# Performance work log

Hardware: AMD Instinct MI355X
Metric: run time of the kernel (lower is better)

## Reference

```python
import jax, jax.numpy as jnp
import numpy as np

B, CIN, H, W = 4, 512, 63, 63
CI, CO = 256, 512  # dim_inter, dim_out
K = 9              # adaptive pool output size; H % K == 0 so pool is exact 7x7 avg
BN_EPS = 1e-5


def conv1x1(x, w, b):
    # x: [B,C,H,W], w: [O,C], b: [O]
    return jnp.einsum('bchw,oc->bohw', x, w) + b[None, :, None, None]


def bn_eval(x, gamma, beta):
    # eval-mode BatchNorm2d with running_mean=0, running_var=1
    s = gamma / jnp.sqrt(jnp.asarray(1.0 + BN_EPS, x.dtype))
    return x * s[None, :, None, None] + beta[None, :, None, None]


def setup_inputs() -> dict:
    key = jax.random.key(0)
    ks = jax.random.split(key, 11)
    sc = 0.02
    return {
        'data_input': jax.random.normal(ks[0], (B, CIN, H, W), jnp.float32),
        'Wk': jax.random.normal(ks[1], (CI, CIN), jnp.float32) * sc,
        'bk': jnp.zeros((CI,), jnp.float32),
        'gamma': 1.0 + 0.1 * jax.random.normal(ks[2], (CI,), jnp.float32),
        'beta': 0.1 * jax.random.normal(ks[3], (CI,), jnp.float32),
        'Wv': jax.random.normal(ks[4], (CI, CIN), jnp.float32) * sc,
        'bv': jnp.zeros((CI,), jnp.float32),
        'Wv2': jax.random.normal(ks[5], (CI, CI), jnp.float32) * sc,
        'bv2': jnp.zeros((CI,), jnp.float32),
        'Ww': jax.random.normal(ks[6], (CO, CI), jnp.float32) * sc,  # note: torch init is 0; randomized for a non-trivial baseline
        'bw': jnp.zeros((CO,), jnp.float32),
    }


def reference(data_input, Wk, bk, gamma, beta, Wv, bv, Wv2, bv2, Ww, bw):
    x = data_input
    scale = jnp.asarray(CI ** (-0.5), x.dtype)

    value = conv1x1(x, Wv, bv)                       # [B,CI,H,W]
    # AdaptiveAvgPool2d(9) with H,W divisible by 9 -> exact block average
    v2 = value.reshape(B, CI, K, H // K, K, W // K).mean(axis=(3, 5))  # [B,CI,9,9]
    v2 = conv1x1(v2, Wv2, bv2).reshape(B, CI, K * K)  # [B,CI,81]

    qk = bn_eval(conv1x1(x, Wk, bk), gamma, beta).reshape(B, CI, -1)  # shared query/key [B,CI,N]
    v = value.reshape(B, CI, -1)                      # [B,CI,N]

    # sim_map = softmax(Q^T K / sqrt(C)) over keys -> [B,N,N]
    sim = jax.nn.softmax(jnp.einsum('bcn,bcm->bnm', qk, qk) * scale, axis=-1)
    # sim_map_value = softmax(V^T V2 / sqrt(C)) -> [B,N,81]
    simv = jax.nn.softmax(jnp.einsum('bcn,bck->bnk', v, v2) * scale, axis=-1)

    sim_new = jnp.einsum('bnm,bmk->bnk', sim, simv)   # [B,N,81]
    ctx = jnp.einsum('bnk,bck->bcn', sim_new, v2).reshape(B, CI, H, W)
    return conv1x1(ctx, Ww, bw)                       # [B,CO,H,W]
```

## Files before the change

### kernel.cpp

```cpp
#include <hip/hip_runtime.h>
#include <hip/hip_bf16.h>

#define BB 4
#define CINsz 512
#define HH 63
#define NN 3969
#define NPAD 4032
#define NPAD2 4096
#define CI 256
#define CO 512
#define NK 81
#define NKP 96
#define SCALE 0.0625f
#define BN_EPS 1e-5f
#define NSPLIT 4

typedef __bf16 bf16x8 __attribute__((ext_vector_type(8)));
typedef float f32x4 __attribute__((ext_vector_type(4)));
typedef unsigned short us8 __attribute__((ext_vector_type(8)));
typedef unsigned short us4 __attribute__((ext_vector_type(4)));

#define MFMA16(a, b, c) __builtin_amdgcn_mfma_f32_16x16x32_bf16((a), (b), (c), 0, 0, 0)

__device__ inline unsigned short f2bf(float x) {
    union { float f; unsigned int u; } v; v.f = x;
    unsigned int r = v.u + 0x7FFF + ((v.u >> 16) & 1);
    return (unsigned short)(r >> 16);
}
__device__ inline float bf2f(unsigned short u) {
    union { unsigned int u; float f; } v; v.u = ((unsigned int)u) << 16;
    return v.f;
}

__device__ inline void gll16(const void* g, void* l) {
    __builtin_amdgcn_global_load_lds(
        (const __attribute__((address_space(1))) unsigned int*)g,
        (__attribute__((address_space(3))) unsigned int*)l, 16, 0, 0);
}

__global__ __launch_bounds__(256) void k_prep(
    const float* __restrict__ Wk, const float* __restrict__ bk,
    const float* __restrict__ gamma, const float* __restrict__ beta,
    const float* __restrict__ Wv, const float* __restrict__ bv,
    const float* __restrict__ Wv2, const float* __restrict__ Ww,
    unsigned short* __restrict__ Wkv, float* __restrict__ bias2,
    unsigned short* __restrict__ Wv2b, unsigned short* __restrict__ Wwb,
    unsigned short* __restrict__ qkbf)
{
    int idx = blockIdx.x * 256 + threadIdx.x;
    if (idx < 512 * 512) {
        int o = idx >> 9, c = idx & 511;
        float v;
        if (o < 256) { float s = gamma[o] * rsqrtf(1.f + BN_EPS); v = Wk[(size_t)o * 512 + c] * s; }
        else v = Wv[(size_t)(o - 256) * 512 + c];
        Wkv[idx] = f2bf(v);
        if (c == 0) {
            bias2[o] = (o < 256) ? (bk[o] * (gamma[o] * rsqrtf(1.f + BN_EPS)) + beta[o]) : bv[o - 256];
        }
    } else if (idx < 512 * 512 + 256 * 256) {
        int j = idx - 512 * 512;
        Wv2b[j] = f2bf(Wv2[j]);
    } else if (idx < 512 * 512 + 256 * 256 + 512 * 256) {
        int j = idx - 512 * 512 - 256 * 256;
        Wwb[j] = f2bf(Ww[j]);
    } else if (idx < 512 * 512 + 256 * 256 + 512 * 256 + 8192) {
        int j = idx - (512 * 512 + 256 * 256 + 512 * 256);
        int b = j >> 11, rem = j & 2047;
        us8 z = (us8){0, 0, 0, 0, 0, 0, 0, 0};
        *reinterpret_cast<us8*>(&qkbf[(size_t)b * NPAD2 * CI + (size_t)NPAD * CI + rem * 8]) = z;
    }
}

__global__ __launch_bounds__(256) void k_qkv(const float* __restrict__ x,
                                             const unsigned short* __restrict__ Wkv,
                                             const float* __restrict__ bias2,
                                             unsigned short* __restrict__ qkbf,
                                             unsigned short* __restrict__ value)
{
    int b = blockIdx.y;
    int nbase = blockIdx.x * 32;
    int tid = threadIdx.x, w = tid >> 6, lane = tid & 63, lg = lane >> 4, lr = lane & 15;
    int half = w >> 1;
    int o_off = half * 256;
    int nloc = (w & 1) * 16 + lr;

    __shared__ unsigned short xs[256 * 34];
    __shared__ unsigned short wk[512 * 32];

    f32x4 acc[16];
#pragma unroll
    for (int t = 0; t < 16; ++t) acc[t] = (f32x4){0.f, 0.f, 0.f, 0.f};

    int n_l = tid & 31, cg = tid >> 5;
    int n_g = nbase + n_l;
    bool nok = n_g < NN;

    for (int h = 0; h < 2; ++h) {
        __syncthreads();
        const float* xsrc = x + ((size_t)b * CINsz + h * 256 + cg) * NN + n_g;
#pragma unroll
        for (int i = 0; i < 32; ++i) {
            int cl = cg + i * 8;
            xs[cl * 34 + n_l] = nok ? f2bf(xsrc[(size_t)(i * 8) * NN]) : (unsigned short)0;
        }
        for (int s8 = 0; s8 < 8; ++s8) {
            int c0 = (h * 8 + s8) * 32;
            __syncthreads();
#pragma unroll
            for (int j = 0; j < 8; ++j) {
                int o = w * 128 + j * 16 + (lane >> 2);
                int slot = (lane & 3) ^ (o & 3);
                gll16(Wkv + (size_t)o * CINsz + c0 + slot * 8,
                      &wk[(w * 128 + j * 16) * 32]);
            }
            __syncthreads();
            bf16x8 af;
#pragma unroll
            for (int j2 = 0; j2 < 8; ++j2)
                af[j2] = __builtin_bit_cast(__bf16, xs[(s8 * 32 + lg * 8 + j2) * 34 + nloc]);
            __builtin_amdgcn_s_setprio(1);
#pragma unroll
            for (int t = 0; t < 16; ++t) {
                int o_loc = o_off + t * 16 + lr;
                bf16x8 bf = *reinterpret_cast<const bf16x8*>(
                    &wk[o_loc * 32 + ((lg ^ (o_loc & 3)) << 3)]);
                acc[t] = MFMA16(af, bf, acc[t]);
            }
            __builtin_amdgcn_s_setprio(0);
        }
    }
    if (half == 0) {
        unsigned short* dst = qkbf + (size_t)b * NPAD2 * CI;
#pragma unroll
        for (int t = 0; t < 16; ++t) {
            int o = t * 16 + lr;
            float bsum = bias2[o];
#pragma unroll
            for (int r = 0; r < 4; ++r) {
                int n = nbase + (w & 1) * 16 + lg * 4 + r;
                dst[(size_t)n * CI + o] = f2bf((acc[t][r] + bsum) * 0.25f);
            }
        }
    } else {
        unsigned short* dst = value + (size_t)b * NPAD * CI;
#pragma unroll
        for (int t = 0; t < 16; ++t) {
            int o = t * 16 + lr;
            float bsum = bias2[256 + o];
#pragma unroll
            for (int r = 0; r < 4; ++r) {
                int n = nbase + (w & 1) * 16 + lg * 4 + r;
                dst[(size_t)n * CI + o] = f2bf(acc[t][r] + bsum);
            }
        }
    }
}

__global__ __launch_bounds__(256) void k_pool(const unsigned short* __restrict__ value,
                                              unsigned short* __restrict__ pooled)
{
    int b = blockIdx.y, k = blockIdx.x, c = threadIdx.x;
    unsigned short* dst = pooled + ((size_t)b * NKP + k) * CI + c;
    if (k >= NK) { *dst = 0; return; }
    int ky = k / 9, kx = k % 9;
    const unsigned short* vb = value + (size_t)b * NPAD * CI + c;
    float s = 0.f;
#pragma unroll
    for (int y = 0; y < 7; ++y)
#pragma unroll
        for (int xx = 0; xx < 7; ++xx) {
            int n = (ky * 7 + y) * HH + kx * 7 + xx;
            s += bf2f(vb[(size_t)n * CI]);
        }
    *dst = f2bf(s * (1.f / 49.f));
}

__global__ __launch_bounds__(256) void k_v2(const unsigned short* __restrict__ pooled,
                                            const unsigned short* __restrict__ Wv2b,
                                            const float* __restrict__ bv2,
                                            unsigned short* __restrict__ v2f)
{
    int b = blockIdx.y;
    int tid = threadIdx.x, w = tid >> 6, lane = tid & 63, lg = lane >> 4, lr = lane & 15;
    int ot = blockIdx.x * 4 + w;
    const unsigned short* pb = pooled + (size_t)b * NKP * CI + lg * 8;
    const unsigned short* wb = Wv2b + (size_t)(ot * 16 + lr) * CI + lg * 8;
    f32x4 acc[6];
#pragma unroll
    for (int kt = 0; kt < 6; ++kt) acc[kt] = (f32x4){0.f, 0.f, 0.f, 0.f};
#pragma unroll
    for (int s = 0; s < 8; ++s) {
        bf16x8 bfw = *reinterpret_cast<const bf16x8*>(wb + s * 32);
#pragma unroll
        for (int kt = 0; kt < 6; ++kt) {
            bf16x8 af = *reinterpret_cast<const bf16x8*>(pb + (size_t)(kt * 16 + lr) * CI + s * 32);
            acc[kt] = MFMA16(af, bfw, acc[kt]);
        }
    }
    float bias = bv2[ot * 16 + lr];
#pragma unroll
    for (int kt = 0; kt < 6; ++kt)
#pragma unroll
        for (int r = 0; r < 4; ++r)
            v2f[((size_t)b * NKP + kt * 16 + lg * 4 + r) * CI + ot * 16 + lr] = f2bf(acc[kt][r] + bias);
}

__global__ __launch_bounds__(256) void k_Z(const unsigned short* __restrict__ Wwb,
                                           const unsigned short* __restrict__ v2f,
                                           unsigned short* __restrict__ Zt)
{
    int b = blockIdx.y;
    int tid = threadIdx.x, w = tid >> 6, lane = tid & 63, lg = lane >> 4, lr = lane & 15;
    int ot = blockIdx.x * 4 + w;
    const unsigned short* wb = Wwb + (size_t)(ot * 16 + lr) * CI + lg * 8;
    const unsigned short* vb = v2f + (size_t)b * NKP * CI + lg * 8;
    f32x4 acc[6];
#pragma unroll
    for (int kt = 0; kt < 6; ++kt) acc[kt] = (f32x4){0.f, 0.f, 0.f, 0.f};
#pragma unroll
    for (int s = 0; s < 8; ++s) {
        bf16x8 af = *reinterpret_cast<const bf16x8*>(wb + s * 32);
#pragma unroll
        for (int kt = 0; kt < 6; ++kt) {
            bf16x8 bfv = *reinterpret_cast<const bf16x8*>(vb + (size_t)(kt * 16 + lr) * CI + s * 32);
            acc[kt] = MFMA16(af, bfv, acc[kt]);
        }
    }
#pragma unroll
    for (int kt = 0; kt < 6; ++kt)
#pragma unroll
        for (int r = 0; r < 4; ++r)
            Zt[((size_t)b * CO + ot * 16 + lg * 4 + r) * NKP + kt * 16 + lr] = f2bf(acc[kt][r]);
}

__global__ __launch_bounds__(256) void k_simv(const unsigned short* __restrict__ value,
                                              const unsigned short* __restrict__ v2f,
                                              unsigned short* __restrict__ svT)
{
    int b = blockIdx.y;
    int tid = threadIdx.x, w = tid >> 6, lane = tid & 63, lg = lane >> 4, lr = lane & 15;
    int n0 = blockIdx.x * 64 + w * 16;

    __shared__ unsigned short sv[96 * 256];

    const unsigned short* v2base = v2f + (size_t)b * NKP * CI;
#pragma unroll
    for (int j = 0; j < 12; ++j) {
        int L = w * 12 + j;
        int row = 2 * L + (lane >> 5);
        int c_hw = ((lane & 31) * 8) ^ ((row & 7) << 3);
        gll16(v2base + (size_t)row * CI + c_hw, &sv[2 * L * 256]);
    }
    __syncthreads();

    const unsigned short* vrow = value + ((size_t)b * NPAD + n0 + lr) * CI + lg * 8;
    f32x4 acc[6];
#pragma unroll
    for (int kt = 0; kt < 6; ++kt) acc[kt] = (f32x4){0.f, 0.f, 0.f, 0.f};
#pragma unroll
    for (int s = 0; s < 8; ++s) {
        bf16x8 af = *reinterpret_cast<const bf16x8*>(vrow + s * 32);
        __builtin_amdgcn_s_setprio(1);
#pragma unroll
        for (int kt = 0; kt < 6; ++kt) {
            int row = kt * 16 + lr;
            bf16x8 bfv = *reinterpret_cast<const bf16x8*>(
                &sv[row * 256 + ((s * 32 + lg * 8) ^ ((row & 7) << 3))]);
            acc[kt] = MFMA16(af, bfv, acc[kt]);
        }
        __builtin_amdgcn_s_setprio(0);
    }
#pragma unroll
    for (int kt = 0; kt < 6; ++kt) {
        bool bad = (kt * 16 + lr) >= NK;
#pragma unroll
        for (int r = 0; r < 4; ++r) acc[kt][r] = bad ? -1e30f : acc[kt][r] * SCALE;
    }
#pragma unroll
    for (int r = 0; r < 4; ++r) {
        float m = acc[0][r];
#pragma unroll
        for (int kt = 1; kt < 6; ++kt) m = fmaxf(m, acc[kt][r]);
#pragma unroll
        for (int off = 1; off < 16; off <<= 1) m = fmaxf(m, __shfl_xor(m, off));
        float p[6], sum = 0.f;
#pragma unroll
        for (int kt = 0; kt < 6; ++kt) { p[kt] = __expf(acc[kt][r] - m); sum += p[kt]; }
#pragma unroll
        for (int off = 1; off < 16; off <<= 1) sum += __shfl_xor(sum, off);
        float inv = 1.f / sum;
#pragma unroll
        for (int kt = 0; kt < 6; ++kt) acc[kt][r] = p[kt] * inv;
    }
#pragma unroll
    for (int kt = 0; kt < 6; ++kt) {
        us4 pk;
#pragma unroll
        for (int r = 0; r < 4; ++r) pk[r] = f2bf(acc[kt][r]);
        if (kt * 16 + lr == 81) { pk[0] = pk[1] = pk[2] = pk[3] = 0x3F80; }
        *reinterpret_cast<us4*>(&svT[((size_t)b * NKP + kt * 16 + lr) * NPAD + n0 + lg * 4]) = pk;
    }
}

__global__ __launch_bounds__(256, 2) void k_flash(const unsigned short* __restrict__ qkbf,
                                                  const unsigned short* __restrict__ svT,
                                                  unsigned short* __restrict__ part_acc,
                                                  float* __restrict__ part_ml)
{
    int bid = blockIdx.x;
    int b = bid & 3;
    int rest = bid >> 2;
    int qg = rest & 31;
    int s_id = rest >> 5;
    int lo = s_id * 16;
    int hi = lo + 16 > 63 ? 63 : lo + 16;
    int tid = threadIdx.x, w = tid >> 6, lane = tid & 63, lg = lane >> 4, lr = lane & 15;
    int q0 = qg * 128 + w * 16;

    __shared__ unsigned short k_lds[2][64 * 256];
    __shared__ unsigned short sv_lds[96 * 64];

    const unsigned short* qkb = qkbf + (size_t)b * NPAD2 * CI;
    const unsigned short* svb = svT + (size_t)b * NKP * NPAD;

    bf16x8 qa[2][8];
#pragma unroll
    for (int u = 0; u < 2; ++u)
#pragma unroll
        for (int s = 0; s < 8; ++s)
            qa[u][s] = *reinterpret_cast<const bf16x8*>(
                qkb + (size_t)(q0 + u * 64 + lr) * CI + s * 32 + lg * 8);

    f32x4 acc[2][6];
#pragma unroll
    for (int u = 0; u < 2; ++u)
#pragma unroll
        for (int jt = 0; jt < 6; ++jt) acc[u][jt] = (f32x4){0.f, 0.f, 0.f, 0.f};
    float m_run[2][4];
#pragma unroll
    for (int u = 0; u < 2; ++u)
#pragma unroll
        for (int r = 0; r < 4; ++r) m_run[u][r] = -1e30f;

    auto stageK = [&](int t, int bi) {
#pragma unroll
        for (int j = 0; j < 8; ++j) {
            int r = w * 16 + j * 2 + (lane >> 5);
            int c_hw = ((lane & 31) * 8) ^ ((r & 7) << 3);
            gll16(qkb + (size_t)(t * 64 + r) * CI + c_hw,
                  &k_lds[bi][(w * 16 + j * 2) * 256]);
        }
    };
    auto stageSV = [&](int t) {
#pragma unroll
        for (int j = 0; j < 3; ++j) {
            int k = w * 24 + j * 8 + (lane >> 3);
            int m_hw = ((lane & 7) * 8) ^ ((k & 7) << 3);
            gll16(svb + (size_t)k * NPAD + t * 64 + m_hw,
                  &sv_lds[(w * 24 + j * 8) * 64]);
        }
    };

    stageK(lo, 0);
    stageSV(lo);
    __syncthreads();

    for (int t = lo; t < hi; ++t) {
        int bi = (t - lo) & 1;
        int mbase = t * 64;
        if (t + 1 < hi) stageK(t + 1, bi ^ 1);

        f32x4 s_acc[2][4];
#pragma unroll
        for (int u = 0; u < 2; ++u)
#pragma unroll
            for (int tt = 0; tt < 4; ++tt) s_acc[u][tt] = (f32x4){0.f, 0.f, 0.f, 0.f};
        __builtin_amdgcn_s_setprio(1);
#pragma unroll
        for (int s = 0; s < 8; ++s) {
            bf16x8 kf[4];
#pragma unroll
            for (int tt = 0; tt < 4; ++tt) {
                int row = tt * 16 + lr;
                int hw = (s * 32 + lg * 8) ^ ((row & 7) << 3);
                kf[tt] = *reinterpret_cast<const bf16x8*>(&k_lds[bi][row * 256 + hw]);
            }
#pragma unroll
            for (int tt = 0; tt < 4; ++tt) {
                s_acc[0][tt] = MFMA16(qa[0][s], kf[tt], s_acc[0][tt]);
                s_acc[1][tt] = MFMA16(qa[1][s], kf[tt], s_acc[1][tt]);
            }
        }
        __builtin_amdgcn_s_setprio(0);
        __syncthreads();

        unsigned short* pw = &k_lds[bi][w * 2048];
        bool lastTile = (mbase + 64 > NN);
#pragma unroll
        for (int u = 0; u < 2; ++u) {
            if (lastTile) {
#pragma unroll
                for (int tt = 0; tt < 4; ++tt) {
                    bool bad = (mbase + tt * 16 + lr) >= NN;
#pragma unroll
                    for (int r = 0; r < 4; ++r) if (bad) s_acc[u][tt][r] = -1e30f;
                }
            }
            float pmax[4];
#pragma unroll
            for (int r = 0; r < 4; ++r) {
                float m0 = fmaxf(fmaxf(s_acc[u][0][r], s_acc[u][1][r]),
                                 fmaxf(s_acc[u][2][r], s_acc[u][3][r]));
#pragma unroll
                for (int off = 1; off < 16; off <<= 1) m0 = fmaxf(m0, __shfl_xor(m0, off));
                pmax[r] = m0;
            }
            bool ok = (pmax[0] - m_run[u][0] <= 8.f) && (pmax[1] - m_run[u][1] <= 8.f) &&
                      (pmax[2] - m_run[u][2] <= 8.f) && (pmax[3] - m_run[u][3] <= 8.f);
            if (!__all(ok)) {
#pragma unroll
                for (int r = 0; r < 4; ++r) {
                    float mn = fmaxf(m_run[u][r], pmax[r]);
                    float al = __expf(m_run[u][r] - mn);
                    m_run[u][r] = mn;
#pragma unroll
                    for (int jt = 0; jt < 6; ++jt) acc[u][jt][r] *= al;
                }
            }
            unsigned short* pu = pw + u * 1024;
#pragma unroll
            for (int tt = 0; tt < 4; ++tt) {
#pragma unroll
                for (int r = 0; r < 4; ++r) {
                    float p = __expf(s_acc[u][tt][r] - m_run[u][r]);
                    int row = lg * 4 + r, col = tt * 16 + lr;
                    pu[row * 64 + (col ^ ((row & 7) << 3))] = f2bf(p);
                }
            }
        }
        __builtin_amdgcn_s_setprio(1);
#pragma unroll
        for (int kb = 0; kb < 2; ++kb) {
            int hw = kb * 32 + lg * 8;
            int phw = hw ^ ((lr & 7) << 3);
            bf16x8 pa0 = *reinterpret_cast<const bf16x8*>(&pw[lr * 64 + phw]);
            bf16x8 pa1 = *reinterpret_cast<const bf16x8*>(&pw[1024 + lr * 64 + phw]);
#pragma unroll
            for (int jt = 0; jt < 6; ++jt) {
                int cr = jt * 16 + lr;
                bf16x8 svf = *reinterpret_cast<const bf16x8*>(
                    &sv_lds[cr * 64 + (hw ^ ((cr & 7) << 3))]);
                acc[0][jt] = MFMA16(pa0, svf, acc[0][jt]);
                acc[1][jt] = MFMA16(pa1, svf, acc[1][jt]);
            }
        }
        __builtin_amdgcn_s_setprio(0);
        __syncthreads();
        if (t + 1 < hi) stageSV(t + 1);
    }
    int plane = s_id * 4 + b;
    unsigned short* pa_out = part_acc + (size_t)plane * NPAD2 * 96;
    float* ml_out = part_ml + (size_t)plane * 2 * NPAD2;
#pragma unroll
    for (int u = 0; u < 2; ++u)
#pragma unroll
        for (int r = 0; r < 4; ++r) {
            int row = q0 + u * 64 + lg * 4 + r;
#pragma unroll
            for (int jt = 0; jt < 6; ++jt)
                pa_out[(size_t)row * 96 + jt * 16 + lr] = f2bf(acc[u][jt][r]);
            if (lr == 0) ml_out[row] = m_run[u][r];
            if (lr == 1) ml_out[NPAD2 + row] = acc[u][5][r];
        }
}

__global__ __launch_bounds__(256) void k_out(const unsigned short* __restrict__ part_acc,
                                             const float* __restrict__ part_ml,
                                             const unsigned short* __restrict__ Zt,
                                             const float* __restrict__ bw,
                                             float* __restrict__ out)
{
    int b = blockIdx.y;
    int ng = blockIdx.x;
    int tid = threadIdx.x, w = tid >> 6, lane = tid & 63, lg = lane >> 4, lr = lane & 15;

    __shared__ unsigned short sn[64 * 104];

    for (int j = tid; j < 768; j += 256) {
        int row_l = j / 12, ch = j - row_l * 12;
        int row = ng * 64 + row_l;
        float m_s[NSPLIT], l_s[NSPLIT];
        float mg = -1e30f;
#pragma unroll
        for (int s = 0; s < NSPLIT; ++s) {
            const float* ml = part_ml + (size_t)(s * 4 + b) * 2 * NPAD2;
            m_s[s] = ml[row]; l_s[s] = ml[NPAD2 + row];
            mg = fmaxf(mg, m_s[s]);
        }
        float f_s[NSPLIT], denom = 0.f;
#pragma unroll
        for (int s = 0; s < NSPLIT; ++s) { f_s[s] = __expf(m_s[s] - mg); denom += f_s[s] * l_s[s]; }
        float inv = 1.f / denom;
        float a[8];
#pragma unroll
        for (int q = 0; q < 8; ++q) a[q] = 0.f;
#pragma unroll
        for (int s = 0; s < NSPLIT; ++s) {
            us8 v = *reinterpret_cast<const us8*>(
                &part_acc[((size_t)(s * 4 + b) * NPAD2 + row) * 96 + ch * 8]);
#pragma unroll
            for (int q = 0; q < 8; ++q) a[q] += f_s[s] * bf2f(v[q]);
        }
        us8 o;
#pragma unroll
        for (int q = 0; q < 8; ++q) o[q] = f2bf(a[q] * inv);
        if (ch == 10) o[1] = 0;
        *reinterpret_cast<us8*>(&sn[row_l * 104 + ch * 8]) = o;
    }
    __syncthreads();

    for (int og = 0; og < 8; ++og) {
        int o_row = (og * 4 + w) * 16;
        const unsigned short* za = Zt + ((size_t)b * CO + o_row + lr) * NKP + lg * 8;
        bf16x8 az[3];
#pragma unroll
        for (int ks = 0; ks < 3; ++ks) az[ks] = *reinterpret_cast<const bf16x8*>(za + ks * 32);
        f32x4 acc[4];
#pragma unroll
        for (int jn = 0; jn < 4; ++jn) acc[jn] = (f32x4){0.f, 0.f, 0.f, 0.f};
#pragma unroll
        for (int jn = 0; jn < 4; ++jn)
#pragma unroll
            for (int ks = 0; ks < 3; ++ks) {
                bf16x8 bfs = *reinterpret_cast<const bf16x8*>(
                    &sn[(jn * 16 + lr) * 104 + ks * 32 + lg * 8]);
                acc[jn] = MFMA16(az[ks], bfs, acc[jn]);
            }
#pragma unroll
        for (int r = 0; r < 4; ++r) {
            int o = o_row + lg * 4 + r;
            float bias = bw[o];
            float* orow = out + ((size_t)b * CO + o) * NN;
#pragma unroll
            for (int jn = 0; jn < 4; ++jn) {
                int n = ng * 64 + jn * 16 + lr;
                if (n < NN) orow[n] = acc[jn][r] + bias;
            }
        }
    }
}

extern "C" void kernel_launch(void* const* d_in, const int* in_sizes, int n_in,
                              void* d_out, int out_size, void* d_ws, size_t ws_size,
                              hipStream_t stream)
{
    const float* x     = (const float*)d_in[0];
    const float* Wk    = (const float*)d_in[1];
    const float* bk    = (const float*)d_in[2];
    const float* gamma = (const float*)d_in[3];
    const float* beta  = (const float*)d_in[4];
    const float* Wv    = (const float*)d_in[5];
    const float* bv    = (const float*)d_in[6];
    const float* Wv2   = (const float*)d_in[7];
    const float* bv2   = (const float*)d_in[8];
    const float* Ww    = (const float*)d_in[9];
    const float* bw    = (const float*)d_in[10];
    float* out = (float*)d_out;

    char* p = (char*)d_ws;
    unsigned short* qkbf   = (unsigned short*)p; p += (size_t)BB * NPAD2 * CI * 2;
    unsigned short* value  = (unsigned short*)p; p += (size_t)BB * NPAD * CI * 2;
    unsigned short* svT    = (unsigned short*)p; p += (size_t)BB * NKP * NPAD * 2;
    unsigned short* Wkv    = (unsigned short*)p; p += (size_t)512 * 512 * 2;
    unsigned short* Wv2b   = (unsigned short*)p; p += (size_t)256 * 256 * 2;
    unsigned short* Wwb    = (unsigned short*)p; p += (size_t)512 * 256 * 2;
    unsigned short* pooled = (unsigned short*)p; p += (size_t)BB * NKP * CI * 2;
    unsigned short* v2f    = (unsigned short*)p; p += (size_t)BB * NKP * CI * 2;
    unsigned short* Zt     = (unsigned short*)p; p += (size_t)BB * CO * NKP * 2;
    float* bias2           = (float*)p;          p += 512 * 4;
    unsigned short* part_acc = (unsigned short*)p; p += (size_t)16 * NPAD2 * 96 * 2;
    float* part_ml         = (float*)p;          p += (size_t)16 * 2 * NPAD2 * 4;

    k_prep<<<dim3(1826), 256, 0, stream>>>(Wk, bk, gamma, beta, Wv, bv, Wv2, Ww,
                                           Wkv, bias2, Wv2b, Wwb, qkbf);
    k_qkv<<<dim3(126, BB), 256, 0, stream>>>(x, Wkv, bias2, qkbf, value);
    k_pool<<<dim3(NKP, BB), 256, 0, stream>>>(value, pooled);
    k_v2<<<dim3(4, BB), 256, 0, stream>>>(pooled, Wv2b, bv2, v2f);
    k_Z<<<dim3(8, BB), 256, 0, stream>>>(Wwb, v2f, Zt);
    k_simv<<<dim3(63, BB), 256, 0, stream>>>(value, v2f, svT);
    k_flash<<<dim3(512), 256, 0, stream>>>(qkbf, svT, part_acc, part_ml);
    k_out<<<dim3(63, BB), 256, 0, stream>>>(part_acc, part_ml, Zt, bw, out);
}
```

Measured before the change: 158.2 us.

## Single-buffer K tile in LDS with register prefetch to fit three blocks per CU

The flash kernel drops its double-buffered K tile in LDS for a single buffer. The next K tile is now prefetched into registers and written to LDS after the P·V stage, with explicit waitcnt and barrier placement. This cuts LDS per block from about 76KB to 44KB, so launch bounds can rise to 3 blocks per CU for more latency hiding. The cost is 32 extra VGPRs held across the QK compute under a tighter register cap, which risks spills. It also adds an extra LDS write and barrier per tile and a redundant load on the last iteration.

```diff
diff --git a/kernel.cpp b/kernel.cpp
--- a/kernel.cpp
+++ b/kernel.cpp
@@ -302,7 +302,7 @@
     }
 }
 
-__global__ __launch_bounds__(256, 2) void k_flash(const unsigned short* __restrict__ qkbf,
+__global__ __launch_bounds__(256, 3) void k_flash(const unsigned short* __restrict__ qkbf,
                                                   const unsigned short* __restrict__ svT,
                                                   unsigned short* __restrict__ part_acc,
                                                   float* __restrict__ part_ml)
@@ -317,8 +317,8 @@
     int tid = threadIdx.x, w = tid >> 6, lane = tid & 63, lg = lane >> 4, lr = lane & 15;
     int q0 = qg * 128 + w * 16;
 
-    __shared__ unsigned short k_lds[2][64 * 256];
-    __shared__ unsigned short sv_lds[96 * 64];
+    __shared__ __align__(16) unsigned short k_lds[64 * 256];
+    __shared__ __align__(16) unsigned short sv_lds[96 * 64];
 
     const unsigned short* qkb = qkbf + (size_t)b * NPAD2 * CI;
     const unsigned short* svb = svT + (size_t)b * NKP * NPAD;
@@ -342,33 +342,31 @@
 #pragma unroll
         for (int r = 0; r < 4; ++r) m_run[u][r] = -1e30f;
 
-    auto stageK = [&](int t, int bi) {
+#pragma unroll
+    for (int j = 0; j < 8; ++j) {
+        int r = w * 16 + j * 2 + (lane >> 5);
+        int c_hw = ((lane & 31) * 8) ^ ((r & 7) << 3);
+        gll16(qkb + (size_t)(lo * 64 + r) * CI + c_hw, &k_lds[(w * 16 + j * 2) * 256]);
+    }
+#pragma unroll
+    for (int j = 0; j < 3; ++j) {
+        int k = w * 24 + j * 8 + (lane >> 3);
+        int m_hw = ((lane & 7) * 8) ^ ((k & 7) << 3);
+        gll16(svb + (size_t)k * NPAD + lo * 64 + m_hw, &sv_lds[(w * 24 + j * 8) * 64]);
+    }
+    __syncthreads();
+
+    for (int t = lo; t < hi; ++t) {
+        int mbase = t * 64;
+        int tn = (t + 1 < hi) ? t + 1 : hi - 1;
+
+        us8 kreg[8];
 #pragma unroll
         for (int j = 0; j < 8; ++j) {
             int r = w * 16 + j * 2 + (lane >> 5);
             int c_hw = ((lane & 31) * 8) ^ ((r & 7) << 3);
-            gll16(qkb + (size_t)(t * 64 + r) * CI + c_hw,
-                  &k_lds[bi][(w * 16 + j * 2) * 256]);
-        }
-    };
-    auto stageSV = [&](int t) {
-#pragma unroll
-        for (int j = 0; j < 3; ++j) {
-            int k = w * 24 + j * 8 + (lane >> 3);
-            int m_hw = ((lane & 7) * 8) ^ ((k & 7) << 3);
-            gll16(svb + (size_t)k * NPAD + t * 64 + m_hw,
-                  &sv_lds[(w * 24 + j * 8) * 64]);
-        }
-    };
-
-    stageK(lo, 0);
-    stageSV(lo);
-    __syncthreads();
-
-    for (int t = lo; t < hi; ++t) {
-        int bi = (t - lo) & 1;
-        int mbase = t * 64;
-        if (t + 1 < hi) stageK(t + 1, bi ^ 1);
+            kreg[j] = *reinterpret_cast<const us8*>(qkb + (size_t)(tn * 64 + r) * CI + c_hw);
+        }
 
         f32x4 s_acc[2][4];
 #pragma unroll
@@ -383,7 +381,7 @@
             for (int tt = 0; tt < 4; ++tt) {
                 int row = tt * 16 + lr;
                 int hw = (s * 32 + lg * 8) ^ ((row & 7) << 3);
-                kf[tt] = *reinterpret_cast<const bf16x8*>(&k_lds[bi][row * 256 + hw]);
+                kf[tt] = *reinterpret_cast<const bf16x8*>(&k_lds[row * 256 + hw]);
             }
 #pragma unroll
             for (int tt = 0; tt < 4; ++tt) {
@@ -392,9 +390,11 @@
             }
         }
         __builtin_amdgcn_s_setprio(0);
-        __syncthreads();
-
-        unsigned short* pw = &k_lds[bi][w * 2048];
+        asm volatile("s_waitcnt vmcnt(8) lgkmcnt(0)" ::: "memory");
+        __builtin_amdgcn_s_barrier();
+        __builtin_amdgcn_sched_barrier(0);
+
+        unsigned short* pw = &k_lds[w * 2048];
         bool lastTile = (mbase + 64 > NN);
 #pragma unroll
         for (int u = 0; u < 2; ++u) {
@@ -456,7 +456,19 @@
         }
         __builtin_amdgcn_s_setprio(0);
         __syncthreads();
-        if (t + 1 < hi) stageSV(t + 1);
+
+#pragma unroll
+        for (int j = 0; j < 3; ++j) {
+            int k = w * 24 + j * 8 + (lane >> 3);
+            int m_hw = ((lane & 7) * 8) ^ ((k & 7) << 3);
+            gll16(svb + (size_t)k * NPAD + tn * 64 + m_hw, &sv_lds[(w * 24 + j * 8) * 64]);
+        }
+#pragma unroll
+        for (int j = 0; j < 8; ++j)
+            *reinterpret_cast<us8*>(&k_lds[(w * 16 + j * 2) * 256 + lane * 8]) = kreg[j];
+        asm volatile("s_waitcnt lgkmcnt(0)" ::: "memory");
+        __builtin_amdgcn_s_barrier();
+        __builtin_amdgcn_sched_barrier(0);
     }
     int plane = s_id * 4 + b;
     unsigned short* pa_out = part_acc + (size_t)plane * NPAD2 * 96;
```

Measured after the change: 347.8 us. +119.8%, slower.
